# Performance work log

Measured on AMD Instinct MI355X. Metric: run time of the kernel, lower is better.

## Reference

```python
import jax, jax.numpy as jnp
import numpy as np

NB, NA, NC, NH, NW = 16, 5, 80, 64, 64
MAXT = 50            # max gt boxes per image
THRESH = 0.6         # ignore threshold
NOOBJ_SCALE = 1.0
OBJ_SCALE = 5.0
NTOT = NB * NA * NH * NW


def _iou_cwh(b1, b2):
    """IoU for center-format (x,y,w,h) boxes, broadcasting over leading dims."""
    x1, y1, w1, h1 = (b1[..., i] for i in range(4))
    x2, y2, w2, h2 = (b2[..., i] for i in range(4))
    cw = jnp.minimum(x1 + 0.5 * w1, x2 + 0.5 * w2) - jnp.maximum(x1 - 0.5 * w1, x2 - 0.5 * w2)
    ch = jnp.minimum(y1 + 0.5 * h1, y2 + 0.5 * h2) - jnp.maximum(y1 - 0.5 * h1, y2 - 0.5 * h2)
    inter = jnp.maximum(cw, 0.0) * jnp.maximum(ch, 0.0)
    union = w1 * h1 + w2 * h2 - inter
    return jnp.where(inter > 0, inter / union, 0.0)


def setup_inputs() -> dict:
    key = jax.random.key(0)
    k1, k2, k3, k4 = jax.random.split(key, 4)
    output = jax.random.normal(k1, (NB, NA * (5 + NC), NH, NW), jnp.float32)
    nval = 20  # valid boxes per image; rest zero (loop-break semantics)
    cls = jax.random.randint(k2, (NB, nval), 0, NC).astype(jnp.float32)
    xy = jax.random.uniform(k3, (NB, nval, 2), minval=0.05, maxval=0.95)
    wh = jax.random.uniform(k4, (NB, nval, 2), minval=0.05, maxval=0.30)
    boxes = jnp.concatenate([cls[..., None], xy, wh], axis=-1)      # [NB,nval,5]
    pad = jnp.zeros((NB, MAXT - nval, 5), jnp.float32)
    target = jnp.concatenate([boxes, pad], axis=1).reshape(NB, MAXT * 5)
    anchors = jnp.array([[0.57273, 0.677385], [1.87446, 2.06253], [3.33843, 5.47434],
                         [7.88282, 3.52778], [9.77052, 9.16828]], jnp.float32)
    return {"output": output, "target": target, "anchors": anchors}


def reference(output, target, anchors):
    target = jax.lax.stop_gradient(target)  # target.detach() in torch
    out = output.reshape(NB, NA, 5 + NC, NH, NW)
    tx = jax.nn.sigmoid(out[:, :, 0])
    ty = jax.nn.sigmoid(out[:, :, 1])
    tw, th = out[:, :, 2], out[:, :, 3]
    conf = jax.nn.sigmoid(out[:, :, 4])                   # [B,A,H,W]
    cls_logits = jnp.moveaxis(out[:, :, 5:], 2, -1)       # [B,A,H,W,C]

    aw, ah = anchors[:, 0], anchors[:, 1]
    # decoded pred boxes, detached (only used for target building, as in torch)
    pred = jax.lax.stop_gradient(jnp.stack([
        tx + jnp.arange(NW, dtype=jnp.float32)[None, None, None, :],
        ty + jnp.arange(NH, dtype=jnp.float32)[None, None, :, None],
        jnp.exp(tw) * aw[None, :, None, None],
        jnp.exp(th) * ah[None, :, None, None]], axis=-1))  # [B,A,H,W,4]
    anchors_sg = jax.lax.stop_gradient(anchors)
    aw_sg, ah_sg = anchors_sg[:, 0], anchors_sg[:, 1]

    tb = target.reshape(NB, MAXT, 5)
    # torch breaks at first box with x==0 -> cumulative validity
    valid = jnp.cumprod((tb[:, :, 1] != 0).astype(jnp.int32), axis=1) > 0  # [B,T]
    gcls = tb[:, :, 0]
    gx, gw = tb[:, :, 1] * NW, tb[:, :, 3] * NW
    gy, gh = tb[:, :, 2] * NH, tb[:, :, 4] * NH
    gt = jnp.stack([gx, gy, gw, gh], axis=-1)             # [B,T,4]

    # ignore mask: max IoU of each pred box against all valid gt
    ious = _iou_cwh(gt[:, :, None, None, None, :], pred[:, None])  # [B,T,A,H,W]
    ious = jnp.where(valid[:, :, None, None, None], ious, 0.0)
    conf_mask = jnp.where(ious.max(axis=1) > THRESH, 0.0, NOOBJ_SCALE)  # [B,A,H,W]

    # anchor assignment: IoU of (0,0,gw,gh) vs (0,0,aw,ah) -> argmax anchor
    inter = jnp.minimum(gw[..., None], aw_sg) * jnp.minimum(gh[..., None], ah_sg)
    union = gw[..., None] * gh[..., None] + aw_sg * ah_sg - inter
    best_n = jnp.argmax(inter / union, axis=-1)           # [B,T]

    gi = jnp.clip(gx.astype(jnp.int32), 0, NW - 1)
    gj = jnp.clip(gy.astype(jnp.int32), 0, NH - 1)
    cell = best_n * (NH * NW) + gj * NW + gi              # [B,T] index in A*H*W
    mpred = jnp.take_along_axis(pred.reshape(NB, NA * NH * NW, 4), cell[:, :, None], axis=1)
    iou_best = _iou_cwh(gt, mpred)                        # [B,T]

    flat = cell + jnp.arange(NB)[:, None] * (NA * NH * NW)
    flat = jnp.where(valid, flat, NTOT).reshape(-1)       # out-of-range -> dropped
    fv = lambda v: v.reshape(-1)
    gw_s = jnp.where(valid, gw, 1.0)
    gh_s = jnp.where(valid, gh, 1.0)
    awb, ahb = aw_sg[best_n], ah_sg[best_n]

    cls_mask = jnp.zeros(NTOT, jnp.float32).at[flat].set(1.0, mode='drop')
    conf_mask = conf_mask.reshape(-1).at[flat].set(OBJ_SCALE, mode='drop')
    # seen < 12800 -> tcoord xy default 0.5, coord_mask all ones
    t0 = jnp.full((NTOT,), 0.5).at[flat].set(fv(gx - gi.astype(jnp.float32)), mode='drop')
    t1 = jnp.full((NTOT,), 0.5).at[flat].set(fv(gy - gj.astype(jnp.float32)), mode='drop')
    t2 = jnp.zeros(NTOT).at[flat].set(fv(jnp.log(gw_s / awb)), mode='drop')
    t3 = jnp.zeros(NTOT).at[flat].set(fv(jnp.log(gh_s / ahb)), mode='drop')
    tconf = jnp.zeros(NTOT).at[flat].set(fv(iou_best), mode='drop')
    tcls = jnp.zeros(NTOT, jnp.int32).at[flat].set(fv(gcls.astype(jnp.int32)), mode='drop')

    coord = jnp.stack([tx, ty, tw, th], axis=0).reshape(4, NTOT)
    tcoord = jnp.stack([t0, t1, t2, t3], axis=0)
    loss_coord = 0.5 * jnp.sum((coord - tcoord) ** 2)     # coord_mask == 1 everywhere
    loss_conf = 0.5 * jnp.sum(conf_mask * (conf.reshape(-1) - tconf) ** 2)
    logp = jax.nn.log_softmax(cls_logits, axis=-1).reshape(NTOT, NC)
    ce = -jnp.take_along_axis(logp, tcls[:, None], axis=1)[:, 0]
    loss_cls = jnp.sum(ce * cls_mask)
    return loss_coord + loss_conf + loss_cls
```

## Files before the change

kernel.cpp:

```cpp
#include <hip/hip_runtime.h>
#include <math.h>

constexpr int kNB   = 16;
constexpr int kNA   = 5;
constexpr int kNC   = 80;
constexpr int kNH   = 64;
constexpr int kNW   = 64;
constexpr int kMAXT = 50;
constexpr int kCH    = 5 + kNC;
constexpr int kPLANE = kNH * kNW;
constexpr int kCELLS_B = kNA * kPLANE;
constexpr int kBLK  = 256;
constexpr int kBPB  = kCELLS_B / kBLK;
constexpr int kGRID = kNB * kBPB;
constexpr float kOBJ = 5.0f;

constexpr int kRECF = 16;

__device__ __forceinline__ float frcp(float x) { return __builtin_amdgcn_rcpf(x); }
__device__ __forceinline__ float fsig(float x) { return frcp(1.0f + __expf(-x)); }

__global__ __launch_bounds__(256) void k_fused(const float* __restrict__ out,
                                               const float* __restrict__ target,
                                               const float* __restrict__ anchors,
                                               float* __restrict__ partials) {
    __shared__ __align__(16) float srec[kMAXT * kRECF];
    __shared__ int snv;
    __shared__ float wred[4];

    const int tid  = threadIdx.x;
    const int wave = tid >> 6;
    const int lane = tid & 63;
    const int b    = blockIdx.x / kBPB;
    const int t_ce = blockIdx.x % kBPB;

    const int cidx = t_ce * kBLK + tid;
    const int a    = cidx / kPLANE;
    const int remp = cidx & (kPLANE - 1);
    const int i    = remp & (kNW - 1), j = remp >> 6;
    const float* ob = out + ((size_t)(b * kNA + a) * kCH) * kPLANE + remp;
    float o0 = ob[0];
    float o1 = ob[kPLANE];
    float o2 = ob[2 * kPLANE];
    float o3 = ob[3 * kPLANE];
    float o4 = ob[4 * kPLANE];

    float ceV0 = 0.f, ceV1 = -INFINITY, ceLt = 0.f;
    bool doCE = false;

    if (wave == 0) {
        int t = lane;
        float c0 = 0.f, x = 0.f, y = 0.f, w = 0.f, h = 0.f;
        if (t < kMAXT) {
            const float* tp = target + (b * kMAXT + t) * 5;
            c0 = tp[0]; x = tp[1]; y = tp[2]; w = tp[3]; h = tp[4];
        }
        unsigned long long m = __ballot(x != 0.0f);
        int nv = (int)__builtin_ctzll(~m);
        if (t == 0) snv = nv;

        if (t < nv) {
            float gx = x * kNW, gy = y * kNH, gw = w * kNW, gh = h * kNH;
            int bn = 0; float best = -1.0f;
            for (int n = 0; n < kNA; ++n) {
                float aw_ = anchors[2 * n], ah_ = anchors[2 * n + 1];
                float inter = fminf(gw, aw_) * fminf(gh, ah_);
                float uni = gw * gh + aw_ * ah_ - inter;
                float r = inter / uni;
                if (r > best) { best = r; bn = n; }
            }
            float aw = anchors[2 * bn], ah = anchors[2 * bn + 1];
            int gi = (int)gx; gi = gi < 0 ? 0 : (gi > kNW - 1 ? kNW - 1 : gi);
            int gj = (int)gy; gj = gj < 0 ? 0 : (gj > kNH - 1 ? kNH - 1 : gj);
            int cell = bn * kPLANE + gj * kNW + gi;

            const float* mb = out + ((size_t)(b * kNA + bn) * kCH) * kPLANE + gj * kNW + gi;
            float px = fsig(mb[0]) + (float)gi;
            float py = fsig(mb[kPLANE]) + (float)gj;
            float pw = __expf(mb[2 * kPLANE]) * aw;
            float ph = __expf(mb[3 * kPLANE]) * ah;
            float cw  = fminf(gx + 0.5f * gw, px + 0.5f * pw) - fmaxf(gx - 0.5f * gw, px - 0.5f * pw);
            float chh = fminf(gy + 0.5f * gh, py + 0.5f * ph) - fmaxf(gy - 0.5f * gh, py - 0.5f * ph);
            float inter = fmaxf(cw, 0.f) * fmaxf(chh, 0.f);
            float uni = gw * gh + pw * ph - inter;
            float iou = (inter > 0.f) ? inter / uni : 0.f;

            float* r = srec + t * kRECF;
            r[0]  = gx - 0.5f * gw;  r[1]  = gx + 0.5f * gw;
            r[2]  = gy - 0.5f * gh;  r[3]  = gy + 0.5f * gh;
            r[4]  = 0.6f * gw * gh;  r[5]  = __int_as_float(cell);
            r[8]  = gx - (float)gi;  r[9]  = gy - (float)gj;
            r[10] = __logf(gw / aw); r[11] = __logf(gh / ah);
            r[12] = iou;             r[13] = c0;
        }
    } else if (wave == 1) {
        int t = lane;
        float c0 = 0.f, x = 0.f, y = 0.f, w = 0.f, h = 0.f;
        if (t < kMAXT) {
            const float* tp = target + (b * kMAXT + t) * 5;
            c0 = tp[0]; x = tp[1]; y = tp[2]; w = tp[3]; h = tp[4];
        }
        unsigned long long m = __ballot(x != 0.0f);
        int nv = (int)__builtin_ctzll(~m);

        int cell = -1;
        if (t < nv) {
            float gx = x * kNW, gy = y * kNH, gw = w * kNW, gh = h * kNH;
            int bn = 0; float best = -1.0f;
            for (int n = 0; n < kNA; ++n) {
                float aw_ = anchors[2 * n], ah_ = anchors[2 * n + 1];
                float inter = fminf(gw, aw_) * fminf(gh, ah_);
                float uni = gw * gh + aw_ * ah_ - inter;
                float r = inter / uni;
                if (r > best) { best = r; bn = n; }
            }
            int gi = (int)gx; gi = gi < 0 ? 0 : (gi > kNW - 1 ? kNW - 1 : gi);
            int gj = (int)gy; gj = gj < 0 ? 0 : (gj > kNH - 1 ? kNH - 1 : gj);
            cell = bn * kPLANE + gj * kNW + gi;
        }
        int   cellT = __shfl(cell, t_ce & 63, 64);
        float c0T   = __shfl(c0,   t_ce & 63, 64);
        unsigned long long dup = __ballot(t > t_ce && cell == cellT && cell >= 0);
        doCE = (t_ce < nv) && (dup == 0ull);
        if (doCE) {
            int bn = cellT >> 12, pix = cellT & (kPLANE - 1);
            int tcls = (int)c0T;
            const float* lg = out + ((size_t)(b * kNA + bn) * kCH + 5) * kPLANE + pix;
            ceV0 = lg[(size_t)lane * kPLANE];
            if (lane < kNC - 64) ceV1 = lg[(size_t)(64 + lane) * kPLANE];
            ceLt = lg[(size_t)tcls * kPLANE];
        }
    }
    __syncthreads();
    const int nv = snv;

    float tx   = fsig(o0);
    float ty   = fsig(o1);
    float tw   = o2;
    float th   = o3;
    float conf = fsig(o4);

    float aw = anchors[2 * a], ah = anchors[2 * a + 1];
    float pw = __expf(tw) * aw, ph = __expf(th) * ah;
    float px = tx + (float)i, py = ty + (float)j;
    float px1 = px - 0.5f * pw, px2 = px + 0.5f * pw;
    float py1 = py - 0.5f * ph, py2 = py + 0.5f * ph;
    float p06 = 0.6f * pw * ph;
    int mycell = a * kPLANE + remp;

    float flag = -INFINITY;
    int match = -1;
    for (int t = 0; t < nv; ++t) {
        const float4 bx = *reinterpret_cast<const float4*>(srec + t * kRECF);
        const float2 gc = *reinterpret_cast<const float2*>(srec + t * kRECF + 4);
        float cw  = fminf(bx.y, px2) - fmaxf(bx.x, px1);
        float chh = fminf(bx.w, py2) - fmaxf(bx.z, py1);
        float inter = fmaxf(cw, 0.f) * fmaxf(chh, 0.f);
        flag = fmaxf(flag, fmaf(1.6f, inter, -gc.x));
        match = (__float_as_int(gc.y) == mycell) ? t : match;
    }

    float t0 = 0.5f, t1 = 0.5f, t2 = 0.f, t3 = 0.f, tconf = 0.f, cmask;
    if (match >= 0) {
        const float4 tt = *reinterpret_cast<const float4*>(srec + match * kRECF + 8);
        t0 = tt.x; t1 = tt.y; t2 = tt.z; t3 = tt.w;
        tconf = srec[match * kRECF + 12];
        cmask = kOBJ;
    } else {
        cmask = (flag > p06) ? 0.f : 1.f;
    }

    float dx = tx - t0, dy = ty - t1, dw = tw - t2, dh = th - t3, dc = conf - tconf;
    float loss = 0.5f * (dx * dx + dy * dy + dw * dw + dh * dh)
               + 0.5f * cmask * dc * dc;

    if (wave == 1 && doCE) {
        float mx = fmaxf(ceV0, ceV1);
        #pragma unroll
        for (int off = 32; off > 0; off >>= 1) mx = fmaxf(mx, __shfl_xor(mx, off, 64));
        float s = __expf(ceV0 - mx) + ((lane < kNC - 64) ? __expf(ceV1 - mx) : 0.f);
        #pragma unroll
        for (int off = 32; off > 0; off >>= 1) s += __shfl_xor(s, off, 64);
        if (lane == 0) loss += __logf(s) + mx - ceLt;
    }

    #pragma unroll
    for (int off = 32; off > 0; off >>= 1) loss += __shfl_down(loss, off, 64);
    if (lane == 0) wred[wave] = loss;
    __syncthreads();
    if (tid == 0)
        partials[blockIdx.x] = wred[0] + wred[1] + wred[2] + wred[3];
}

__global__ __launch_bounds__(64) void k_final(const float* __restrict__ partials,
                                              float* __restrict__ outv) {
    float s = 0.f;
    for (int k = threadIdx.x; k < kGRID; k += 64) s += partials[k];
    #pragma unroll
    for (int off = 32; off > 0; off >>= 1) s += __shfl_xor(s, off, 64);
    if (threadIdx.x == 0) outv[0] = s;
}

extern "C" void kernel_launch(void* const* d_in, const int* in_sizes, int n_in,
                              void* d_out, int out_size, void* d_ws, size_t ws_size,
                              hipStream_t stream) {
    const float* output  = (const float*)d_in[0];
    const float* target  = (const float*)d_in[1];
    const float* anchors = (const float*)d_in[2];

    float* partials = (float*)d_ws;

    k_fused<<<kGRID, kBLK, 0, stream>>>(output, target, anchors, partials);
    k_final<<<1, 64, 0, stream>>>(partials, (float*)d_out);
}
```

Measured before the change: 16.94 us.

## Precompute per-image target records in a prologue kernel and atomically accumulate loss

Moves the per-image ground-truth processing (anchor matching, IoU, duplicate-cell ownership) out of every block of the main kernel into a small 16-block prologue kernel that writes records to global memory. The main kernel then just copies the records into shared memory instead of redoing the target work in two waves per block. The final reduction kernel is replaced by a float atomicAdd per block into the output, which the prologue zeroes. Kernel count is unchanged, but the main kernel now depends on a serial tiny prologue, and float atomics make the summation order nondeterministic.

```diff
diff --git a/kernel.cpp b/kernel.cpp
--- a/kernel.cpp
+++ b/kernel.cpp
@@ -16,25 +16,91 @@
 constexpr float kOBJ = 5.0f;
 
 constexpr int kRECF = 16;
+constexpr int kRECB = kMAXT * kRECF;
 
 __device__ __forceinline__ float frcp(float x) { return __builtin_amdgcn_rcpf(x); }
 __device__ __forceinline__ float fsig(float x) { return frcp(1.0f + __expf(-x)); }
 
+__global__ __launch_bounds__(64) void k_targets(const float* __restrict__ out,
+                                                const float* __restrict__ target,
+                                                const float* __restrict__ anchors,
+                                                float* __restrict__ recG,
+                                                int* __restrict__ nvArr,
+                                                float* __restrict__ outv) {
+    const int b = blockIdx.x, t = threadIdx.x;
+    if (b == 0 && t == 0) outv[0] = 0.f;
+
+    float c0 = 0.f, x = 0.f, y = 0.f, w = 0.f, h = 0.f;
+    if (t < kMAXT) {
+        const float* tp = target + (b * kMAXT + t) * 5;
+        c0 = tp[0]; x = tp[1]; y = tp[2]; w = tp[3]; h = tp[4];
+    }
+    unsigned long long m = __ballot(x != 0.0f);
+    int nv = (int)__builtin_ctzll(~m);
+    if (t == 0) nvArr[b] = nv;
+
+    const bool act = (t < nv);
+    int cell = -1, gi = 0, gj = 0, bn = 0;
+    float gx = 0, gy = 0, gw = 0, gh = 0, aw = 1.f, ah = 1.f;
+    if (act) {
+        gx = x * kNW; gy = y * kNH; gw = w * kNW; gh = h * kNH;
+        float best = -1.0f;
+        for (int n = 0; n < kNA; ++n) {
+            float aw_ = anchors[2 * n], ah_ = anchors[2 * n + 1];
+            float inter = fminf(gw, aw_) * fminf(gh, ah_);
+            float uni = gw * gh + aw_ * ah_ - inter;
+            float r = inter / uni;
+            if (r > best) { best = r; bn = n; }
+        }
+        aw = anchors[2 * bn]; ah = anchors[2 * bn + 1];
+        gi = (int)gx; gi = gi < 0 ? 0 : (gi > kNW - 1 ? kNW - 1 : gi);
+        gj = (int)gy; gj = gj < 0 ? 0 : (gj > kNH - 1 ? kNH - 1 : gj);
+        cell = bn * kPLANE + gj * kNW + gi;
+    }
+    bool owner = act;
+    for (int t2 = 0; t2 < kMAXT; ++t2) {
+        int c2 = __shfl(cell, t2, 64);
+        if (act && t2 > t && c2 == cell) owner = false;
+    }
+    if (act) {
+        const float* mb = out + ((size_t)(b * kNA + bn) * kCH) * kPLANE + gj * kNW + gi;
+        float px = fsig(mb[0]) + (float)gi;
+        float py = fsig(mb[kPLANE]) + (float)gj;
+        float pw = __expf(mb[2 * kPLANE]) * aw;
+        float ph = __expf(mb[3 * kPLANE]) * ah;
+        float cw  = fminf(gx + 0.5f * gw, px + 0.5f * pw) - fmaxf(gx - 0.5f * gw, px - 0.5f * pw);
+        float chh = fminf(gy + 0.5f * gh, py + 0.5f * ph) - fmaxf(gy - 0.5f * gh, py - 0.5f * ph);
+        float inter = fmaxf(cw, 0.f) * fmaxf(chh, 0.f);
+        float uni = gw * gh + pw * ph - inter;
+        float iou = (inter > 0.f) ? inter / uni : 0.f;
+
+        float* r = recG + b * kRECB + t * kRECF;
+        r[0]  = gx - 0.5f * gw;  r[1]  = gx + 0.5f * gw;
+        r[2]  = gy - 0.5f * gh;  r[3]  = gy + 0.5f * gh;
+        r[4]  = 0.6f * gw * gh;  r[5]  = __int_as_float(cell);
+        r[6]  = owner ? 1.f : 0.f; r[7] = 0.f;
+        r[8]  = gx - (float)gi;  r[9]  = gy - (float)gj;
+        r[10] = __logf(gw / aw); r[11] = __logf(gh / ah);
+        r[12] = iou;             r[13] = c0;
+        r[14] = 0.f;             r[15] = 0.f;
+    }
+}
+
 __global__ __launch_bounds__(256) void k_fused(const float* __restrict__ out,
-                                               const float* __restrict__ target,
                                                const float* __restrict__ anchors,
-                                               float* __restrict__ partials) {
-    __shared__ __align__(16) float srec[kMAXT * kRECF];
-    __shared__ int snv;
+                                               const float* __restrict__ recG,
+                                               const int* __restrict__ nvArr,
+                                               float* __restrict__ outv) {
+    __shared__ __align__(16) float srec[kRECB];
     __shared__ float wred[4];
 
     const int tid  = threadIdx.x;
     const int wave = tid >> 6;
     const int lane = tid & 63;
     const int b    = blockIdx.x / kBPB;
-    const int t_ce = blockIdx.x % kBPB;
-
-    const int cidx = t_ce * kBLK + tid;
+    const int blkb = blockIdx.x % kBPB;
+
+    const int cidx = blkb * kBLK + tid;
     const int a    = cidx / kPLANE;
     const int remp = cidx & (kPLANE - 1);
     const int i    = remp & (kNW - 1), j = remp >> 6;
@@ -45,94 +111,23 @@
     float o3 = ob[3 * kPLANE];
     float o4 = ob[4 * kPLANE];
 
+    const int nv = nvArr[b];
+
+    for (int k = tid; k < kRECB; k += kBLK) srec[k] = recG[b * kRECB + k];
+    __syncthreads();
+
     float ceV0 = 0.f, ceV1 = -INFINITY, ceLt = 0.f;
     bool doCE = false;
-
-    if (wave == 0) {
-        int t = lane;
-        float c0 = 0.f, x = 0.f, y = 0.f, w = 0.f, h = 0.f;
-        if (t < kMAXT) {
-            const float* tp = target + (b * kMAXT + t) * 5;
-            c0 = tp[0]; x = tp[1]; y = tp[2]; w = tp[3]; h = tp[4];
-        }
-        unsigned long long m = __ballot(x != 0.0f);
-        int nv = (int)__builtin_ctzll(~m);
-        if (t == 0) snv = nv;
-
-        if (t < nv) {
-            float gx = x * kNW, gy = y * kNH, gw = w * kNW, gh = h * kNH;
-            int bn = 0; float best = -1.0f;
-            for (int n = 0; n < kNA; ++n) {
-                float aw_ = anchors[2 * n], ah_ = anchors[2 * n + 1];
-                float inter = fminf(gw, aw_) * fminf(gh, ah_);
-                float uni = gw * gh + aw_ * ah_ - inter;
-                float r = inter / uni;
-                if (r > best) { best = r; bn = n; }
-            }
-            float aw = anchors[2 * bn], ah = anchors[2 * bn + 1];
-            int gi = (int)gx; gi = gi < 0 ? 0 : (gi > kNW - 1 ? kNW - 1 : gi);
-            int gj = (int)gy; gj = gj < 0 ? 0 : (gj > kNH - 1 ? kNH - 1 : gj);
-            int cell = bn * kPLANE + gj * kNW + gi;
-
-            const float* mb = out + ((size_t)(b * kNA + bn) * kCH) * kPLANE + gj * kNW + gi;
-            float px = fsig(mb[0]) + (float)gi;
-            float py = fsig(mb[kPLANE]) + (float)gj;
-            float pw = __expf(mb[2 * kPLANE]) * aw;
-            float ph = __expf(mb[3 * kPLANE]) * ah;
-            float cw  = fminf(gx + 0.5f * gw, px + 0.5f * pw) - fmaxf(gx - 0.5f * gw, px - 0.5f * pw);
-            float chh = fminf(gy + 0.5f * gh, py + 0.5f * ph) - fmaxf(gy - 0.5f * gh, py - 0.5f * ph);
-            float inter = fmaxf(cw, 0.f) * fmaxf(chh, 0.f);
-            float uni = gw * gh + pw * ph - inter;
-            float iou = (inter > 0.f) ? inter / uni : 0.f;
-
-            float* r = srec + t * kRECF;
-            r[0]  = gx - 0.5f * gw;  r[1]  = gx + 0.5f * gw;
-            r[2]  = gy - 0.5f * gh;  r[3]  = gy + 0.5f * gh;
-            r[4]  = 0.6f * gw * gh;  r[5]  = __int_as_float(cell);
-            r[8]  = gx - (float)gi;  r[9]  = gy - (float)gj;
-            r[10] = __logf(gw / aw); r[11] = __logf(gh / ah);
-            r[12] = iou;             r[13] = c0;
-        }
-    } else if (wave == 1) {
-        int t = lane;
-        float c0 = 0.f, x = 0.f, y = 0.f, w = 0.f, h = 0.f;
-        if (t < kMAXT) {
-            const float* tp = target + (b * kMAXT + t) * 5;
-            c0 = tp[0]; x = tp[1]; y = tp[2]; w = tp[3]; h = tp[4];
-        }
-        unsigned long long m = __ballot(x != 0.0f);
-        int nv = (int)__builtin_ctzll(~m);
-
-        int cell = -1;
-        if (t < nv) {
-            float gx = x * kNW, gy = y * kNH, gw = w * kNW, gh = h * kNH;
-            int bn = 0; float best = -1.0f;
-            for (int n = 0; n < kNA; ++n) {
-                float aw_ = anchors[2 * n], ah_ = anchors[2 * n + 1];
-                float inter = fminf(gw, aw_) * fminf(gh, ah_);
-                float uni = gw * gh + aw_ * ah_ - inter;
-                float r = inter / uni;
-                if (r > best) { best = r; bn = n; }
-            }
-            int gi = (int)gx; gi = gi < 0 ? 0 : (gi > kNW - 1 ? kNW - 1 : gi);
-            int gj = (int)gy; gj = gj < 0 ? 0 : (gj > kNH - 1 ? kNH - 1 : gj);
-            cell = bn * kPLANE + gj * kNW + gi;
-        }
-        int   cellT = __shfl(cell, t_ce & 63, 64);
-        float c0T   = __shfl(c0,   t_ce & 63, 64);
-        unsigned long long dup = __ballot(t > t_ce && cell == cellT && cell >= 0);
-        doCE = (t_ce < nv) && (dup == 0ull);
-        if (doCE) {
-            int bn = cellT >> 12, pix = cellT & (kPLANE - 1);
-            int tcls = (int)c0T;
-            const float* lg = out + ((size_t)(b * kNA + bn) * kCH + 5) * kPLANE + pix;
-            ceV0 = lg[(size_t)lane * kPLANE];
-            if (lane < kNC - 64) ceV1 = lg[(size_t)(64 + lane) * kPLANE];
-            ceLt = lg[(size_t)tcls * kPLANE];
-        }
-    }
-    __syncthreads();
-    const int nv = snv;
+    if (wave == 1 && blkb < nv && srec[blkb * kRECF + 6] != 0.f) {
+        doCE = true;
+        int cell = __float_as_int(srec[blkb * kRECF + 5]);
+        int bn = cell >> 12, pix = cell & (kPLANE - 1);
+        int tcls = (int)srec[blkb * kRECF + 13];
+        const float* lg = out + ((size_t)(b * kNA + bn) * kCH + 5) * kPLANE + pix;
+        ceV0 = lg[(size_t)lane * kPLANE];
+        if (lane < kNC - 64) ceV1 = lg[(size_t)(64 + lane) * kPLANE];
+        ceLt = lg[(size_t)tcls * kPLANE];
+    }
 
     float tx   = fsig(o0);
     float ty   = fsig(o1);
@@ -146,7 +141,6 @@
     float px1 = px - 0.5f * pw, px2 = px + 0.5f * pw;
     float py1 = py - 0.5f * ph, py2 = py + 0.5f * ph;
     float p06 = 0.6f * pw * ph;
-    int mycell = a * kPLANE + remp;
 
     float flag = -INFINITY;
     int match = -1;
@@ -157,7 +151,7 @@
         float chh = fminf(bx.w, py2) - fmaxf(bx.z, py1);
         float inter = fmaxf(cw, 0.f) * fmaxf(chh, 0.f);
         flag = fmaxf(flag, fmaf(1.6f, inter, -gc.x));
-        match = (__float_as_int(gc.y) == mycell) ? t : match;
+        match = (__float_as_int(gc.y) == cidx) ? t : match;
     }
 
     float t0 = 0.5f, t1 = 0.5f, t2 = 0.f, t3 = 0.f, tconf = 0.f, cmask;
@@ -174,7 +168,7 @@
     float loss = 0.5f * (dx * dx + dy * dy + dw * dw + dh * dh)
                + 0.5f * cmask * dc * dc;
 
-    if (wave == 1 && doCE) {
+    if (doCE) {
         float mx = fmaxf(ceV0, ceV1);
         #pragma unroll
         for (int off = 32; off > 0; off >>= 1) mx = fmaxf(mx, __shfl_xor(mx, off, 64));
@@ -189,16 +183,7 @@
     if (lane == 0) wred[wave] = loss;
     __syncthreads();
     if (tid == 0)
-        partials[blockIdx.x] = wred[0] + wred[1] + wred[2] + wred[3];
-}
-
-__global__ __launch_bounds__(64) void k_final(const float* __restrict__ partials,
-                                              float* __restrict__ outv) {
-    float s = 0.f;
-    for (int k = threadIdx.x; k < kGRID; k += 64) s += partials[k];
-    #pragma unroll
-    for (int off = 32; off > 0; off >>= 1) s += __shfl_xor(s, off, 64);
-    if (threadIdx.x == 0) outv[0] = s;
+        atomicAdd(outv, wred[0] + wred[1] + wred[2] + wred[3]);
 }
 
 extern "C" void kernel_launch(void* const* d_in, const int* in_sizes, int n_in,
@@ -208,8 +193,9 @@
     const float* target  = (const float*)d_in[1];
     const float* anchors = (const float*)d_in[2];
 
-    float* partials = (float*)d_ws;
-
-    k_fused<<<kGRID, kBLK, 0, stream>>>(output, target, anchors, partials);
-    k_final<<<1, 64, 0, stream>>>(partials, (float*)d_out);
+    float* recG  = (float*)d_ws;
+    int*   nvArr = (int*)(recG + kNB * kRECB);
+
+    k_targets<<<kNB, 64, 0, stream>>>(output, target, anchors, recG, nvArr, (float*)d_out);
+    k_fused<<<kGRID, kBLK, 0, stream>>>(output, anchors, recG, nvArr, (float*)d_out);
 }
```

Result: slower. 29.54 us (+74.4%).
